# Optimization experiments

Measured on AMD Instinct MI355X. Metric: run time of the kernel, lower is better.

The kernel has to match this reference:

```python
import jax, jax.numpy as jnp
import numpy as np

N_NODES = 100000
N_EDGES = 1600000
N_GRAPHS = 64
NUM_FEATURES = 512
NUM_CLASSES = 10


def setup_inputs() -> dict:
    key = jax.random.key(0)
    ks = jax.random.split(key, 8)
    x = jax.random.normal(ks[0], (N_NODES, NUM_FEATURES), dtype=jnp.float32)
    edge_index = jax.random.randint(ks[1], (2, N_EDGES), 0, N_NODES, dtype=jnp.int32)
    batch = jnp.sort(jax.random.randint(ks[2], (N_NODES,), 0, N_GRAPHS, dtype=jnp.int32))
    def init_w(k, fin, fout):
        return jax.random.normal(k, (fin, fout), dtype=jnp.float32) * (1.0 / np.sqrt(fin))
    W1 = init_w(ks[3], NUM_FEATURES, 128)
    W2 = init_w(ks[4], 128, 64)
    W3 = init_w(ks[5], 64, 32)
    Wfc = init_w(ks[6], 32, NUM_CLASSES)
    return {
        "x": x, "edge_index": edge_index, "batch": batch,
        "W1": W1, "b1": jnp.zeros((128,), jnp.float32),
        "W2": W2, "b2": jnp.zeros((64,), jnp.float32),
        "W3": W3, "b3": jnp.zeros((32,), jnp.float32),
        "Wfc": Wfc, "bfc": jnp.zeros((NUM_CLASSES,), jnp.float32),
    }


def _gcn_conv(x, src, dst, norm, W, b):
    # PyG GCNConv: linear first, then normalized neighbor aggregation (with self-loops), then bias.
    h = x @ W                                   # [N, F_out]
    msg = norm[:, None] * h[src]                # gather + scale, [E+N, F_out]
    out = jnp.zeros_like(h).at[dst].add(msg)    # scatter-add to targets
    return out + b


def reference(x, edge_index, batch, W1, b1, W2, b2, W3, b3, Wfc, bfc):
    n = x.shape[0]
    loops = jnp.arange(n, dtype=edge_index.dtype)
    src = jnp.concatenate([edge_index[0], loops])  # source nodes (+ self-loops)
    dst = jnp.concatenate([edge_index[1], loops])  # target nodes (+ self-loops)
    # symmetric normalization D^{-1/2} (A+I) D^{-1/2}; degrees counted at targets
    deg = jnp.zeros((n,), x.dtype).at[dst].add(1.0)
    dinv = jnp.where(deg > 0, jax.lax.rsqrt(deg), 0.0)
    norm = dinv[src] * dinv[dst]                # [E+N]

    h = jax.nn.relu(_gcn_conv(x, src, dst, norm, W1, b1))   # dropout is identity in eval
    h = jax.nn.relu(_gcn_conv(h, src, dst, norm, W2, b2))
    h = jax.nn.relu(_gcn_conv(h, src, dst, norm, W3, b3))

    pooled = jax.ops.segment_max(h, batch, num_segments=N_GRAPHS)  # global max pool per graph
    logits = pooled @ Wfc + bfc
    return jax.nn.log_softmax(logits, axis=1)
```

## Files before the change

### kernel.cpp

```cpp
#include <hip/hip_runtime.h>
#include <hip/hip_bf16.h>


typedef __attribute__((ext_vector_type(8))) short short8;
typedef __attribute__((ext_vector_type(8))) unsigned short ushort8v;
typedef __attribute__((ext_vector_type(4))) float f32x4;

constexpr int NB   = 1024;
constexpr int CAPB = 4096;
constexpr int EPB  = 6400;

__device__ __forceinline__ unsigned short f2bf(float f) {
    __hip_bfloat16 h = __float2bfloat16(f);
    return *(unsigned short*)&h;
}
__device__ __forceinline__ float bfu2f(unsigned short u) {
    unsigned int v = ((unsigned int)u) << 16;
    return __uint_as_float(v);
}

__global__ void init_kernel(int* __restrict__ bcnt, float* __restrict__ pooled) {
    int i = blockIdx.x * 256 + threadIdx.x;
    if (i < NB * 16) bcnt[i] = 0;
    if (i < 64 * 32) pooled[i] = 0.0f;
}

__global__ __launch_bounds__(256) void partition_edges(
        const int* __restrict__ src, const int* __restrict__ dst,
        int* __restrict__ bcnt, unsigned* __restrict__ bucketed, int E) {
    __shared__ unsigned h[NB], rs[NB], cur[NB], gs[NB];
    __shared__ unsigned wtot[4];
    __shared__ unsigned ebuf[EPB];
    __shared__ unsigned short ebkt[EPB];

    const int t = threadIdx.x;
    const int e0 = blockIdx.x * EPB;
    const int nloc = min(EPB, E - e0);

    for (int i = t; i < NB; i += 256) h[i] = 0;
    __syncthreads();

    for (int i = t; i < nloc; i += 256) {
        int d = dst[e0 + i];
        atomicAdd(&h[d >> 7], 1u);
    }
    __syncthreads();

    const unsigned b0 = 4u * t;
    unsigned s0 = h[b0], s1 = h[b0 + 1], s2 = h[b0 + 2], s3 = h[b0 + 3];
    unsigned tsum = s0 + s1 + s2 + s3;
    unsigned scan = tsum;
#pragma unroll
    for (int off = 1; off < 64; off <<= 1) {
        unsigned v = __shfl_up(scan, off, 64);
        if ((t & 63) >= off) scan += v;
    }
    if ((t & 63) == 63) wtot[t >> 6] = scan;
    __syncthreads();
    unsigned woff = 0;
    for (int w = 0; w < (t >> 6); ++w) woff += wtot[w];
    unsigned excl = woff + scan - tsum;
    rs[b0] = excl;                 cur[b0] = excl;
    rs[b0 + 1] = excl + s0;        cur[b0 + 1] = excl + s0;
    rs[b0 + 2] = excl + s0 + s1;   cur[b0 + 2] = excl + s0 + s1;
    rs[b0 + 3] = excl + s0 + s1 + s2; cur[b0 + 3] = excl + s0 + s1 + s2;
    if (s0) gs[b0]     = (unsigned)atomicAdd(&bcnt[(b0) * 16], (int)s0);
    if (s1) gs[b0 + 1] = (unsigned)atomicAdd(&bcnt[(b0 + 1) * 16], (int)s1);
    if (s2) gs[b0 + 2] = (unsigned)atomicAdd(&bcnt[(b0 + 2) * 16], (int)s2);
    if (s3) gs[b0 + 3] = (unsigned)atomicAdd(&bcnt[(b0 + 3) * 16], (int)s3);
    __syncthreads();

    for (int i = t; i < nloc; i += 256) {
        int d = dst[e0 + i];
        int s = src[e0 + i];
        int b = d >> 7;
        unsigned p = atomicAdd(&cur[b], 1u);
        ebuf[p] = ((unsigned)s << 7) | (unsigned)(d & 127);
        ebkt[p] = (unsigned short)b;
    }
    __syncthreads();

    for (int p = t; p < nloc; p += 256) {
        unsigned v = ebuf[p];
        int b = ebkt[p];
        unsigned g = gs[b] + ((unsigned)p - rs[b]);
        if (g < CAPB) bucketed[(size_t)b * CAPB + g] = v;
    }
}

__global__ __launch_bounds__(256) void bucket_csr(
        const unsigned* __restrict__ bucketed, const int* __restrict__ bcnt,
        int* __restrict__ cnt, int* __restrict__ slab, float* __restrict__ dinv, int N) {
    __shared__ int lcnt[128];
    __shared__ unsigned lslab[128 * 64];

    const int b = blockIdx.x;
    const int t = threadIdx.x;
    if (t < 128) lcnt[t] = 0;
    __syncthreads();

    int nE = bcnt[b * 16];
    if (nE > CAPB) nE = CAPB;
    const unsigned* bb = bucketed + (size_t)b * CAPB;
    for (int e = t; e < nE; e += 256) {
        unsigned v = bb[e];
        int ln = v & 127;
        int pos = atomicAdd(&lcnt[ln], 1);
        if (pos < 64) lslab[ln * 64 + pos] = v >> 7;
    }
    __syncthreads();

    const int node0 = b * 128;
    const int nnodes = min(128, N - node0);
    if (nnodes <= 0) return;
    const int tot4 = (nnodes * 64) / 4;
    int4* gout = (int4*)&slab[(size_t)node0 * 64];
    const int4* lin = (const int4*)lslab;
    for (int i = t; i < tot4; i += 256) gout[i] = lin[i];
    if (t < nnodes) {
        int deg = lcnt[t];
        cnt[node0 + t] = deg;
        dinv[node0 + t] = rsqrtf(1.0f + (float)deg);
    }
}

__global__ void wconv(const float* __restrict__ W, unsigned short* __restrict__ Wt,
                      int K, int N) {
    int idx = blockIdx.x * 256 + threadIdx.x;
    if (idx < N * K) {
        int n = idx / K, k = idx % K;
        Wt[idx] = f2bf(W[(size_t)k * N + n]);
    }
}

template <int NOUT, bool A_BF16>
__global__ __launch_bounds__(256) void mfma_gemm(
        const float* __restrict__ Af, const unsigned short* __restrict__ Ab,
        const unsigned short* __restrict__ Wt, const float* __restrict__ dinv,
        unsigned short* __restrict__ C, int M, int K) {
    constexpr int NT = NOUT / 16;
    constexpr int CH = 136;

    __shared__ short As[16 * CH];
    __shared__ short Bs[NT * 4 * CH];

    const int t = threadIdx.x;
    const int w = t >> 6;
    const int lane = t & 63;
    const int row0 = blockIdx.x * 64;

    f32x4 acc[NT];
#pragma unroll
    for (int c = 0; c < NT; ++c) acc[c] = (f32x4){0.f, 0.f, 0.f, 0.f};

    const int ar = t >> 2;
    const int aq = t & 3;
    const int arow = row0 + ar;
    const int a_lds = ((ar >> 4) * 4 + aq) * CH + (ar & 15) * 8;

    const int bn = t >> 1;
    const int bh = t & 1;
    const int b_lds0 = ((bn >> 4) * 4 + 2 * bh) * CH + (bn & 15) * 8;

    for (int k0 = 0; k0 < K; k0 += 32) {
        short8 apack;
        if (A_BF16) {
            if (arow < M) apack = *(const short8*)&Ab[(size_t)arow * K + k0 + aq * 8];
            else apack = (short8){0, 0, 0, 0, 0, 0, 0, 0};
        } else {
            float4 u0 = make_float4(0.f, 0.f, 0.f, 0.f), u1 = u0;
            if (arow < M) {
                const float* ap = Af + (size_t)arow * K + k0 + aq * 8;
                u0 = *(const float4*)ap;
                u1 = *(const float4*)(ap + 4);
            }
            apack[0] = (short)f2bf(u0.x); apack[1] = (short)f2bf(u0.y);
            apack[2] = (short)f2bf(u0.z); apack[3] = (short)f2bf(u0.w);
            apack[4] = (short)f2bf(u1.x); apack[5] = (short)f2bf(u1.y);
            apack[6] = (short)f2bf(u1.z); apack[7] = (short)f2bf(u1.w);
        }
        short8 w0, w1;
        if (t < 2 * NOUT) {
            const unsigned short* wp = Wt + (size_t)bn * K + k0 + 16 * bh;
            w0 = *(const short8*)wp;
            w1 = *(const short8*)(wp + 8);
        }
        __syncthreads();
        *(short8*)&As[a_lds] = apack;
        if (t < 2 * NOUT) {
            *(short8*)&Bs[b_lds0] = w0;
            *(short8*)&Bs[b_lds0 + CH] = w1;
        }
        __syncthreads();

        short8 a = *(short8*)&As[(w * 4 + (lane >> 4)) * CH + (lane & 15) * 8];
#pragma unroll
        for (int c = 0; c < NT; ++c) {
            short8 b = *(short8*)&Bs[(c * 4 + (lane >> 4)) * CH + (lane & 15) * 8];
            acc[c] = __builtin_amdgcn_mfma_f32_16x16x32_bf16(a, b, acc[c], 0, 0, 0);
        }
    }

    const int q = lane >> 4, i = lane & 15;
#pragma unroll
    for (int reg = 0; reg < 4; ++reg) {
        int row = row0 + w * 16 + q * 4 + reg;
        if (row < M) {
            float di = dinv[row];
#pragma unroll
            for (int c = 0; c < NT; ++c)
                C[(size_t)row * NOUT + c * 16 + i] = f2bf(di * acc[c][reg]);
        }
    }
}

template <int F, bool OUT_BF16>
__global__ void gather_relu(const int* __restrict__ cnt, const int* __restrict__ slab,
                            const float* __restrict__ dinv,
                            const unsigned short* __restrict__ hs,
                            const float* __restrict__ bias, void* __restrict__ outv, int N) {
    constexpr int F8 = F / 8;
    constexpr int NPB = 256 / F8;
    const int node = blockIdx.x * NPB + threadIdx.x / F8;
    if (node >= N) return;
    const int lane = threadIdx.x % F8;
    const size_t fo = (size_t)lane * 8;

    float acc[8];
    {
        ushort8v s = *(const ushort8v*)&hs[(size_t)node * F + fo];
#pragma unroll
        for (int i = 0; i < 8; ++i) acc[i] = bfu2f(s[i]);
    }
    int deg = cnt[node];
    if (deg > 64) deg = 64;
    const int* sl = slab + (size_t)node * 64;

    int j = 0;
    for (; j + 8 <= deg; j += 8) {
        int4 a4 = *(const int4*)&sl[j];
        int4 b4 = *(const int4*)&sl[j + 4];
        ushort8v v0 = *(const ushort8v*)&hs[(size_t)a4.x * F + fo];
        ushort8v v1 = *(const ushort8v*)&hs[(size_t)a4.y * F + fo];
        ushort8v v2 = *(const ushort8v*)&hs[(size_t)a4.z * F + fo];
        ushort8v v3 = *(const ushort8v*)&hs[(size_t)a4.w * F + fo];
        ushort8v v4 = *(const ushort8v*)&hs[(size_t)b4.x * F + fo];
        ushort8v v5 = *(const ushort8v*)&hs[(size_t)b4.y * F + fo];
        ushort8v v6 = *(const ushort8v*)&hs[(size_t)b4.z * F + fo];
        ushort8v v7 = *(const ushort8v*)&hs[(size_t)b4.w * F + fo];
#pragma unroll
        for (int i = 0; i < 8; ++i)
            acc[i] += ((bfu2f(v0[i]) + bfu2f(v1[i])) + (bfu2f(v2[i]) + bfu2f(v3[i]))) +
                      ((bfu2f(v4[i]) + bfu2f(v5[i])) + (bfu2f(v6[i]) + bfu2f(v7[i])));
    }
    for (; j + 4 <= deg; j += 4) {
        int4 s4 = *(const int4*)&sl[j];
        ushort8v v0 = *(const ushort8v*)&hs[(size_t)s4.x * F + fo];
        ushort8v v1 = *(const ushort8v*)&hs[(size_t)s4.y * F + fo];
        ushort8v v2 = *(const ushort8v*)&hs[(size_t)s4.z * F + fo];
        ushort8v v3 = *(const ushort8v*)&hs[(size_t)s4.w * F + fo];
#pragma unroll
        for (int i = 0; i < 8; ++i)
            acc[i] += (bfu2f(v0[i]) + bfu2f(v1[i])) + (bfu2f(v2[i]) + bfu2f(v3[i]));
    }
    for (; j < deg; ++j) {
        int s = sl[j];
        ushort8v v = *(const ushort8v*)&hs[(size_t)s * F + fo];
#pragma unroll
        for (int i = 0; i < 8; ++i) acc[i] += bfu2f(v[i]);
    }

    const float di = dinv[node];
    if (OUT_BF16) {
        ushort8v o;
#pragma unroll
        for (int i = 0; i < 8; ++i) o[i] = f2bf(fmaxf(di * acc[i] + bias[fo + i], 0.f));
        *(ushort8v*)&((unsigned short*)outv)[(size_t)node * F + fo] = o;
    } else {
        float ov[8];
#pragma unroll
        for (int i = 0; i < 8; ++i) ov[i] = fmaxf(di * acc[i] + bias[fo + i], 0.f);
        float4* op = (float4*)&((float*)outv)[(size_t)node * F + fo];
        op[0] = make_float4(ov[0], ov[1], ov[2], ov[3]);
        op[1] = make_float4(ov[4], ov[5], ov[6], ov[7]);
    }
}

__global__ void pool_max(const float* __restrict__ h, const int* __restrict__ batch,
                         float* __restrict__ pooled, int N) {
    int t = blockIdx.x * 256 + threadIdx.x;
    int f = t % 32;
    int i0 = (t / 32) * 32;
    if (i0 >= N) return;
    int gcur = -1;
    float vmax = 0.f;
    for (int j = 0; j < 32; ++j) {
        int i = i0 + j;
        if (i >= N) break;
        int g = batch[i];
        if (g != gcur) {
            if (gcur >= 0) atomicMax((int*)&pooled[gcur * 32 + f], __float_as_int(vmax));
            gcur = g;
            vmax = 0.f;
        }
        vmax = fmaxf(vmax, h[(size_t)i * 32 + f]);
    }
    if (gcur >= 0) atomicMax((int*)&pooled[gcur * 32 + f], __float_as_int(vmax));
}

__global__ void head_kernel(const float* __restrict__ pooled, const float* __restrict__ Wfc,
                            const float* __restrict__ bfc, float* __restrict__ out) {
    int g = threadIdx.x;
    float p[32];
#pragma unroll
    for (int f = 0; f < 32; ++f) p[f] = pooled[g * 32 + f];
    float logits[10];
#pragma unroll
    for (int c = 0; c < 10; ++c) {
        float acc = bfc[c];
#pragma unroll
        for (int f = 0; f < 32; ++f) acc += p[f] * Wfc[f * 10 + c];
        logits[c] = acc;
    }
    float m = logits[0];
#pragma unroll
    for (int c = 1; c < 10; ++c) m = fmaxf(m, logits[c]);
    float s = 0.f;
#pragma unroll
    for (int c = 0; c < 10; ++c) s += expf(logits[c] - m);
    float lse = m + logf(s);
#pragma unroll
    for (int c = 0; c < 10; ++c) out[g * 10 + c] = logits[c] - lse;
}

extern "C" void kernel_launch(void* const* d_in, const int* in_sizes, int n_in,
                              void* d_out, int out_size, void* d_ws, size_t ws_size,
                              hipStream_t stream) {
    const float* x   = (const float*)d_in[0];
    const int*   ei  = (const int*)d_in[1];
    const int*   bat = (const int*)d_in[2];
    const float* W1  = (const float*)d_in[3];
    const float* b1  = (const float*)d_in[4];
    const float* W2  = (const float*)d_in[5];
    const float* b2  = (const float*)d_in[6];
    const float* W3  = (const float*)d_in[7];
    const float* b3  = (const float*)d_in[8];
    const float* Wfc = (const float*)d_in[9];
    const float* bfc = (const float*)d_in[10];
    float* out = (float*)d_out;

    const int N = in_sizes[2];
    const int E = in_sizes[1] / 2;
    const int K0 = in_sizes[0] / N;

    const int* src = ei;
    const int* dst = ei + E;

    float* ws = (float*)d_ws;
    float* dinv = ws;
    unsigned short* HS  = (unsigned short*)(ws + N);
    unsigned short* ACT = HS + (size_t)N * 128;
    float* H3 = (float*)ACT;
    float* pooled = (float*)(ACT + (size_t)N * 128);
    unsigned short* Wt1 = (unsigned short*)(pooled + 2048);
    unsigned short* Wt2 = Wt1 + 128 * 512;
    unsigned short* Wt3 = Wt2 + 64 * 128;
    int* cnt = (int*)(Wt3 + 32 * 64);
    int* slab = cnt + N;
    int* bcnt = slab + (size_t)N * 64;
    unsigned* bucketed = (unsigned*)(bcnt + NB * 16);

    const int gb = (N + 63) / 64;
    const int NBUCK = (N + 127) >> 7;

    init_kernel<<<64, 256, 0, stream>>>(bcnt, pooled);
    wconv<<<(128 * 512 + 255) / 256, 256, 0, stream>>>(W1, Wt1, K0, 128);
    wconv<<<(64 * 128 + 255) / 256, 256, 0, stream>>>(W2, Wt2, 128, 64);
    wconv<<<(32 * 64 + 255) / 256, 256, 0, stream>>>(W3, Wt3, 64, 32);

    partition_edges<<<(E + EPB - 1) / EPB, 256, 0, stream>>>(src, dst, bcnt, bucketed, E);
    bucket_csr<<<NBUCK, 256, 0, stream>>>(bucketed, bcnt, cnt, slab, dinv, N);

    const int gath128 = (N + 15) / 16;
    const int gath64  = (N + 31) / 32;
    const int gath32  = (N + 63) / 64;

    mfma_gemm<128, false><<<gb, 256, 0, stream>>>(x, nullptr, Wt1, dinv, HS, N, K0);
    gather_relu<128, true><<<gath128, 256, 0, stream>>>(cnt, slab, dinv, HS, b1, ACT, N);

    mfma_gemm<64, true><<<gb, 256, 0, stream>>>(nullptr, ACT, Wt2, dinv, HS, N, 128);
    gather_relu<64, true><<<gath64, 256, 0, stream>>>(cnt, slab, dinv, HS, b2, ACT, N);

    mfma_gemm<32, true><<<gb, 256, 0, stream>>>(nullptr, ACT, Wt3, dinv, HS, N, 64);
    gather_relu<32, false><<<gath32, 256, 0, stream>>>(cnt, slab, dinv, HS, b3, H3, N);

    pool_max<<<(((N + 31) / 32) * 32 + 255) / 256, 256, 0, stream>>>(H3, bat, pooled, N);
    head_kernel<<<1, 64, 0, stream>>>(pooled, Wfc, bfc, out);
}
```

Baseline: 533.9 us.

## Fuse gather-ReLU with next-layer GEMM and fold pooling into final gather

Each layer's neighbor aggregation and ReLU now writes its activation tile into shared memory, and the next layer's bf16 MFMA GEMM runs on it in the same kernel. This removes the global round trip of intermediate activations and two GEMM launches. The last gather reduces per-graph maxima from shared memory before issuing atomics, replacing the separate pool kernel. The three weight conversions and the init are merged into one setup kernel. The cost is that every gather block reloads the full weight matrix into LDS, and the small 16-row GEMM tiles give less reuse.

```diff
diff --git a/kernel.cpp b/kernel.cpp
--- a/kernel.cpp
+++ b/kernel.cpp
@@ -19,10 +19,26 @@
     return __uint_as_float(v);
 }
 
-__global__ void init_kernel(int* __restrict__ bcnt, float* __restrict__ pooled) {
-    int i = blockIdx.x * 256 + threadIdx.x;
-    if (i < NB * 16) bcnt[i] = 0;
-    if (i < 64 * 32) pooled[i] = 0.0f;
+__global__ void setup_kernel(const float* __restrict__ W1, const float* __restrict__ W2,
+                             const float* __restrict__ W3,
+                             unsigned short* __restrict__ Wt1, unsigned short* __restrict__ Wt2,
+                             unsigned short* __restrict__ Wt3,
+                             int* __restrict__ bcnt, float* __restrict__ pooled) {
+    int t = blockIdx.x * 256 + threadIdx.x;
+    if (t < NB * 16) bcnt[t] = 0;
+    if (t < 64 * 32) pooled[t] = 0.0f;
+    if (t < 128 * 512) {
+        int n = t >> 9, k = t & 511;
+        Wt1[t] = f2bf(W1[(size_t)k * 128 + n]);
+    } else if (t < 128 * 512 + 64 * 128) {
+        int u = t - 128 * 512;
+        int n = u >> 7, k = u & 127;
+        Wt2[u] = f2bf(W2[(size_t)k * 64 + n]);
+    } else if (t < 128 * 512 + 64 * 128 + 32 * 64) {
+        int u = t - (128 * 512 + 64 * 128);
+        int n = u >> 6, k = u & 63;
+        Wt3[u] = f2bf(W3[(size_t)k * 32 + n]);
+    }
 }
 
 __global__ __launch_bounds__(256) void partition_edges(
@@ -60,9 +76,9 @@
     unsigned woff = 0;
     for (int w = 0; w < (t >> 6); ++w) woff += wtot[w];
     unsigned excl = woff + scan - tsum;
-    rs[b0] = excl;                 cur[b0] = excl;
-    rs[b0 + 1] = excl + s0;        cur[b0 + 1] = excl + s0;
-    rs[b0 + 2] = excl + s0 + s1;   cur[b0 + 2] = excl + s0 + s1;
+    rs[b0] = excl;                    cur[b0] = excl;
+    rs[b0 + 1] = excl + s0;           cur[b0 + 1] = excl + s0;
+    rs[b0 + 2] = excl + s0 + s1;      cur[b0 + 2] = excl + s0 + s1;
     rs[b0 + 3] = excl + s0 + s1 + s2; cur[b0 + 3] = excl + s0 + s1 + s2;
     if (s0) gs[b0]     = (unsigned)atomicAdd(&bcnt[(b0) * 16], (int)s0);
     if (s1) gs[b0 + 1] = (unsigned)atomicAdd(&bcnt[(b0 + 1) * 16], (int)s1);
@@ -121,15 +137,6 @@
         int deg = lcnt[t];
         cnt[node0 + t] = deg;
         dinv[node0 + t] = rsqrtf(1.0f + (float)deg);
-    }
-}
-
-__global__ void wconv(const float* __restrict__ W, unsigned short* __restrict__ Wt,
-                      int K, int N) {
-    int idx = blockIdx.x * 256 + threadIdx.x;
-    if (idx < N * K) {
-        int n = idx / K, k = idx % K;
-        Wt[idx] = f2bf(W[(size_t)k * N + n]);
     }
 }
 
@@ -214,19 +221,10 @@
     }
 }
 
-template <int F, bool OUT_BF16>
-__global__ void gather_relu(const int* __restrict__ cnt, const int* __restrict__ slab,
-                            const float* __restrict__ dinv,
-                            const unsigned short* __restrict__ hs,
-                            const float* __restrict__ bias, void* __restrict__ outv, int N) {
-    constexpr int F8 = F / 8;
-    constexpr int NPB = 256 / F8;
-    const int node = blockIdx.x * NPB + threadIdx.x / F8;
-    if (node >= N) return;
-    const int lane = threadIdx.x % F8;
-    const size_t fo = (size_t)lane * 8;
-
-    float acc[8];
+template <int F>
+__device__ __forceinline__ void gather_acc(
+        const int* __restrict__ cnt, const int* __restrict__ slab,
+        const unsigned short* __restrict__ hs, int node, size_t fo, float acc[8]) {
     {
         ushort8v s = *(const ushort8v*)&hs[(size_t)node * F + fo];
 #pragma unroll
@@ -269,43 +267,110 @@
 #pragma unroll
         for (int i = 0; i < 8; ++i) acc[i] += bfu2f(v[i]);
     }
-
-    const float di = dinv[node];
-    if (OUT_BF16) {
-        ushort8v o;
-#pragma unroll
-        for (int i = 0; i < 8; ++i) o[i] = f2bf(fmaxf(di * acc[i] + bias[fo + i], 0.f));
-        *(ushort8v*)&((unsigned short*)outv)[(size_t)node * F + fo] = o;
-    } else {
-        float ov[8];
+}
+
+template <int F, int NOUT>
+__global__ __launch_bounds__(256) void gather_gemm(
+        const int* __restrict__ cnt, const int* __restrict__ slab,
+        const float* __restrict__ dinv, const unsigned short* __restrict__ hs,
+        const float* __restrict__ bias, const unsigned short* __restrict__ Wt,
+        unsigned short* __restrict__ Cout, int N) {
+    constexpr int F8 = F / 8;
+    constexpr int NPB = 256 / F8;
+    constexpr int LDA = F + 8;
+    constexpr int MT = NPB / 16;
+    constexpr int KS = F / 32;
+
+    __shared__ short At[NPB * LDA];
+    __shared__ short Bs[NOUT * LDA];
+
+    const int t = threadIdx.x;
+    const int node0 = blockIdx.x * NPB;
+    const int nl = t / F8;
+    const int lf = t % F8;
+    const int node = node0 + nl;
+    const size_t fo = (size_t)lf * 8;
+
+#pragma unroll
+    for (int idx = t * 8; idx < NOUT * F; idx += 256 * 8) {
+        int r = idx / F, k = idx % F;
+        *(short8*)&Bs[r * LDA + k] = *(const short8*)&Wt[idx];
+    }
+
+    short8 arow = (short8){0, 0, 0, 0, 0, 0, 0, 0};
+    if (node < N) {
+        float acc[8];
+        gather_acc<F>(cnt, slab, hs, node, fo, acc);
+        const float di = dinv[node];
+#pragma unroll
+        for (int i = 0; i < 8; ++i)
+            arow[i] = (short)f2bf(fmaxf(di * acc[i] + bias[fo + i], 0.f));
+    }
+    *(short8*)&At[nl * LDA + lf * 8] = arow;
+    __syncthreads();
+
+    const int w = t >> 6, l = t & 63;
+    const int m = (MT == 1) ? 0 : (w >> 1);
+    const int c = (MT == 1) ? w : (w & 1);
+    f32x4 acc4 = (f32x4){0.f, 0.f, 0.f, 0.f};
+#pragma unroll
+    for (int ks = 0; ks < KS; ++ks) {
+        short8 a = *(short8*)&At[(m * 16 + (l & 15)) * LDA + ks * 32 + (l >> 4) * 8];
+        short8 b = *(short8*)&Bs[(c * 16 + (l & 15)) * LDA + ks * 32 + (l >> 4) * 8];
+        acc4 = __builtin_amdgcn_mfma_f32_16x16x32_bf16(a, b, acc4, 0, 0, 0);
+    }
+    const int q = l >> 4, i = l & 15;
+#pragma unroll
+    for (int reg = 0; reg < 4; ++reg) {
+        int grow = node0 + m * 16 + q * 4 + reg;
+        if (grow < N)
+            Cout[(size_t)grow * NOUT + c * 16 + i] = f2bf(dinv[grow] * acc4[reg]);
+    }
+}
+
+__global__ __launch_bounds__(256) void gather_pool(
+        const int* __restrict__ cnt, const int* __restrict__ slab,
+        const float* __restrict__ dinv, const unsigned short* __restrict__ hs,
+        const float* __restrict__ bias, const int* __restrict__ batch,
+        float* __restrict__ pooled, int N) {
+    constexpr int F = 32, F8 = 4, NPB = 64;
+    __shared__ float P[NPB * 32];
+    __shared__ int gbuf[NPB];
+
+    const int t = threadIdx.x;
+    const int node0 = blockIdx.x * NPB;
+    const int nl = t >> 2, lf = t & 3;
+    const int node = node0 + nl;
+    const size_t fo = (size_t)lf * 8;
+
+    float ov[8] = {0.f, 0.f, 0.f, 0.f, 0.f, 0.f, 0.f, 0.f};
+    if (node < N) {
+        float acc[8];
+        gather_acc<F>(cnt, slab, hs, node, fo, acc);
+        const float di = dinv[node];
 #pragma unroll
         for (int i = 0; i < 8; ++i) ov[i] = fmaxf(di * acc[i] + bias[fo + i], 0.f);
-        float4* op = (float4*)&((float*)outv)[(size_t)node * F + fo];
-        op[0] = make_float4(ov[0], ov[1], ov[2], ov[3]);
-        op[1] = make_float4(ov[4], ov[5], ov[6], ov[7]);
-    }
-}
-
-__global__ void pool_max(const float* __restrict__ h, const int* __restrict__ batch,
-                         float* __restrict__ pooled, int N) {
-    int t = blockIdx.x * 256 + threadIdx.x;
-    int f = t % 32;
-    int i0 = (t / 32) * 32;
-    if (i0 >= N) return;
-    int gcur = -1;
-    float vmax = 0.f;
-    for (int j = 0; j < 32; ++j) {
-        int i = i0 + j;
-        if (i >= N) break;
-        int g = batch[i];
-        if (g != gcur) {
-            if (gcur >= 0) atomicMax((int*)&pooled[gcur * 32 + f], __float_as_int(vmax));
-            gcur = g;
-            vmax = 0.f;
-        }
-        vmax = fmaxf(vmax, h[(size_t)i * 32 + f]);
-    }
-    if (gcur >= 0) atomicMax((int*)&pooled[gcur * 32 + f], __float_as_int(vmax));
+    }
+#pragma unroll
+    for (int i = 0; i < 8; ++i) P[nl * 32 + lf * 8 + i] = ov[i];
+    if (t < NPB) gbuf[t] = (node0 + t < N) ? batch[node0 + t] : -1;
+    __syncthreads();
+
+    if (t < 32) {
+        int gcur = -1;
+        float vmax = 0.f;
+        for (int j = 0; j < NPB; ++j) {
+            int g = gbuf[j];
+            if (g < 0) break;
+            if (g != gcur) {
+                if (gcur >= 0) atomicMax((int*)&pooled[gcur * 32 + t], __float_as_int(vmax));
+                gcur = g;
+                vmax = 0.f;
+            }
+            vmax = fmaxf(vmax, P[j * 32 + t]);
+        }
+        if (gcur >= 0) atomicMax((int*)&pooled[gcur * 32 + t], __float_as_int(vmax));
+    }
 }
 
 __global__ void head_kernel(const float* __restrict__ pooled, const float* __restrict__ Wfc,
@@ -359,9 +424,9 @@
     float* ws = (float*)d_ws;
     float* dinv = ws;
     unsigned short* HS  = (unsigned short*)(ws + N);
-    unsigned short* ACT = HS + (size_t)N * 128;
-    float* H3 = (float*)ACT;
-    float* pooled = (float*)(ACT + (size_t)N * 128);
+    unsigned short* HS2 = HS + (size_t)N * 128;
+    unsigned short* HS3 = HS2 + (size_t)N * 64;
+    float* pooled = (float*)(HS3 + (size_t)N * 32);
     unsigned short* Wt1 = (unsigned short*)(pooled + 2048);
     unsigned short* Wt2 = Wt1 + 128 * 512;
     unsigned short* Wt3 = Wt2 + 64 * 128;
@@ -373,27 +438,21 @@
     const int gb = (N + 63) / 64;
     const int NBUCK = (N + 127) >> 7;
 
-    init_kernel<<<64, 256, 0, stream>>>(bcnt, pooled);
-    wconv<<<(128 * 512 + 255) / 256, 256, 0, stream>>>(W1, Wt1, K0, 128);
-    wconv<<<(64 * 128 + 255) / 256, 256, 0, stream>>>(W2, Wt2, 128, 64);
-    wconv<<<(32 * 64 + 255) / 256, 256, 0, stream>>>(W3, Wt3, 64, 32);
+    setup_kernel<<<(128 * 512 + 64 * 128 + 32 * 64 + 255) / 256, 256, 0, stream>>>(
+        W1, W2, W3, Wt1, Wt2, Wt3, bcnt, pooled);
 
     partition_edges<<<(E + EPB - 1) / EPB, 256, 0, stream>>>(src, dst, bcnt, bucketed, E);
     bucket_csr<<<NBUCK, 256, 0, stream>>>(bucketed, bcnt, cnt, slab, dinv, N);
 
-    const int gath128 = (N + 15) / 16;
-    const int gath64  = (N + 31) / 32;
-    const int gath32  = (N + 63) / 64;
-
     mfma_gemm<128, false><<<gb, 256, 0, stream>>>(x, nullptr, Wt1, dinv, HS, N, K0);
-    gather_relu<128, true><<<gath128, 256, 0, stream>>>(cnt, slab, dinv, HS, b1, ACT, N);
-
-    mfma_gemm<64, true><<<gb, 256, 0, stream>>>(nullptr, ACT, Wt2, dinv, HS, N, 128);
-    gather_relu<64, true><<<gath64, 256, 0, stream>>>(cnt, slab, dinv, HS, b2, ACT, N);
-
-    mfma_gemm<32, true><<<gb, 256, 0, stream>>>(nullptr, ACT, Wt3, dinv, HS, N, 64);
-    gather_relu<32, false><<<gath32, 256, 0, stream>>>(cnt, slab, dinv, HS, b3, H3, N);
-
-    pool_max<<<(((N + 31) / 32) * 32 + 255) / 256, 256, 0, stream>>>(H3, bat, pooled, N);
+
+    gather_gemm<128, 64><<<(N + 15) / 16, 256, 0, stream>>>(
+        cnt, slab, dinv, HS, b1, Wt2, HS2, N);
+
+    gather_gemm<64, 32><<<(N + 31) / 32, 256, 0, stream>>>(
+        cnt, slab, dinv, HS2, b2, Wt3, HS3, N);
+
+    gather_pool<<<(N + 63) / 64, 256, 0, stream>>>(cnt, slab, dinv, HS3, b3, bat, pooled, N);
+
     head_kernel<<<1, 64, 0, stream>>>(pooled, Wfc, bfc, out);
 }
```

Result: faster. 503.2 us (-5.8%).
